# Kernel optimization log

Hardware: AMD Instinct MI355X
Metric: run time of the kernel (lower is better)

Reference implementation:

```python
import jax, jax.numpy as jnp
import numpy as np
from jax import lax

B, T, D, H = 2, 2048, 512, 8
HD = D // H
EPS = 1e-5


def _layernorm(x, g, b):
    m = jnp.mean(x, axis=-1, keepdims=True)
    v = jnp.var(x, axis=-1, keepdims=True)
    return (x - m) / jnp.sqrt(v + EPS) * g + b


def setup_inputs() -> dict:
    key = jax.random.key(0)
    ks = jax.random.split(key, 16)
    s = 0.02
    return {
        "x": jax.random.normal(ks[0], (B, T, D), jnp.float32),
        "pe": jax.random.normal(ks[1], (B, T, D), jnp.float32),
        "conv_w": jax.random.normal(ks[2], (D, D, 3), jnp.float32) * s,   # OIH
        "conv_b": jnp.zeros((D,), jnp.float32),
        "in_proj_w": jax.random.normal(ks[3], (3 * D, D), jnp.float32) * s,
        "in_proj_b": jnp.zeros((3 * D,), jnp.float32),
        "out_proj_w": jax.random.normal(ks[4], (D, D), jnp.float32) * s,
        "out_proj_b": jnp.zeros((D,), jnp.float32),
        "ln1_g": jnp.ones((D,), jnp.float32),
        "ln1_b": jnp.zeros((D,), jnp.float32),
        "w1": jax.random.normal(ks[5], (2 * D, D), jnp.float32) * s,
        "b1": jnp.zeros((2 * D,), jnp.float32),
        "w2": jax.random.normal(ks[6], (D, 2 * D), jnp.float32) * s,
        "b2": jnp.zeros((D,), jnp.float32),
        "ln2_g": jnp.ones((D,), jnp.float32),
        "ln2_b": jnp.zeros((D,), jnp.float32),
    }


def reference(x, pe, conv_w, conv_b, in_proj_w, in_proj_b, out_proj_w,
              out_proj_b, ln1_g, ln1_b, w1, b1, w2, b2, ln2_g, ln2_b):
    Bv, Tv, Dv = x.shape
    window = max(Tv // 4, 1)
    half = window // 2
    idx = jnp.arange(Tv)
    blocked = jnp.abs(idx[:, None] - idx[None, :]) > half  # [T, T]
    mask = jnp.where(blocked, -jnp.inf, 0.0).astype(x.dtype)

    # Conv1d on values: x [B,T,D] -> [B,D,T], kernel3 pad1, back to [B,T,D]
    xT = jnp.transpose(x, (0, 2, 1))
    v_in = lax.conv_general_dilated(xT, conv_w, window_strides=(1,),
                                    padding=((1, 1),),
                                    dimension_numbers=("NCH", "OIH", "NCH"))
    v_in = jnp.transpose(v_in + conv_b[None, :, None], (0, 2, 1))

    # MultiheadAttention(q=x, k=x, v=v_in)
    Wq, Wk, Wv = jnp.split(in_proj_w, 3, axis=0)
    bq, bk, bv = jnp.split(in_proj_b, 3, axis=0)
    q = (x @ Wq.T + bq).reshape(Bv, Tv, H, HD).transpose(0, 2, 1, 3)
    k = (x @ Wk.T + bk).reshape(Bv, Tv, H, HD).transpose(0, 2, 1, 3)
    v = (v_in @ Wv.T + bv).reshape(Bv, Tv, H, HD).transpose(0, 2, 1, 3)

    scores = jnp.einsum("bhqd,bhkd->bhqk", q, k) / np.sqrt(HD).astype(x.dtype)
    scores = scores + mask[None, None]
    attn = jax.nn.softmax(scores, axis=-1)
    ctx = jnp.einsum("bhqk,bhkd->bhqd", attn, v)
    ctx = ctx.transpose(0, 2, 1, 3).reshape(Bv, Tv, Dv)
    attn_out = ctx @ out_proj_w.T + out_proj_b

    h = _layernorm(x + attn_out, ln1_g, ln1_b)
    ffn = jax.nn.relu(h @ w1.T + b1) @ w2.T + b2
    return _layernorm(h + ffn, ln2_g, ln2_b)
```

## Files before the change

### kernel.cpp

```cpp
#include <hip/hip_runtime.h>
#include <cstdint>
#include <cstddef>

static constexpr int kT  = 2048;
static constexpr int kD  = 512;
static constexpr int kB  = 2;
static constexpr int kN  = kB * kT;

using short8 = __attribute__((ext_vector_type(8))) short;
using f32x4  = __attribute__((ext_vector_type(4))) float;
typedef unsigned short ushort;

__device__ inline ushort f2bf(float f) {
  uint32_t u = __builtin_bit_cast(uint32_t, f);
  uint32_t r = (u + 0x7FFFu + ((u >> 16) & 1u)) >> 16;
  return (ushort)r;
}

#define GLOAD_LDS16(g, l)                                         \
  __builtin_amdgcn_global_load_lds(                               \
      (const __attribute__((address_space(1))) void*)(g),         \
      (__attribute__((address_space(3))) void*)(l), 16, 0, 0)

__global__ __launch_bounds__(256) void cast_kernel(
    const float* __restrict__ in, ushort* __restrict__ out, int n4)
{
  for (int t = blockIdx.x * 256 + threadIdx.x; t < n4; t += gridDim.x * 256) {
    float4 v = *reinterpret_cast<const float4*>(&in[(size_t)t * 4]);
    ushort o[4] = {f2bf(v.x), f2bf(v.y), f2bf(v.z), f2bf(v.w)};
    *reinterpret_cast<uint2*>(&out[(size_t)t * 4]) =
        *reinterpret_cast<uint2*>(o);
  }
}

__global__ __launch_bounds__(256) void convw_kernel(
    const float* __restrict__ cw, ushort* __restrict__ wcat)
{
  for (int t = blockIdx.x * 256 + threadIdx.x; t < kD * kD;
       t += gridDim.x * 256) {
    int o = t >> 9, i = t & 511;
    const float* src = &cw[(size_t)(o * kD + i) * 3];
    ushort* dst = &wcat[(size_t)o * (3 * kD) + i];
#pragma unroll
    for (int tap = 0; tap < 3; ++tap) dst[tap * kD] = f2bf(src[tap]);
  }
}

__global__ __launch_bounds__(256) void acat_kernel(
    const ushort* __restrict__ xb, ushort* __restrict__ acat)
{
  const int total = kN * 3 * 64;
  for (int t = blockIdx.x * 256 + threadIdx.x; t < total;
       t += gridDim.x * 256) {
    int m = t / 192, r = t - m * 192;
    int tap = r >> 6, i8 = r & 63;
    int tib = (m & (kT - 1)) + tap - 1;
    uint4 v = {0u, 0u, 0u, 0u};
    if (tib >= 0 && tib < kT)
      v = *reinterpret_cast<const uint4*>(&xb[(size_t)(m + tap - 1) * kD + i8 * 8]);
    *reinterpret_cast<uint4*>(&acat[(size_t)m * (3 * kD) + tap * kD + i8 * 8]) = v;
  }
}

template <typename OutT, int RELU>
__global__ __launch_bounds__(256) void gemm_bf16(
    const ushort* __restrict__ A, const ushort* __restrict__ W,
    const float* __restrict__ bias, OutT* __restrict__ C,
    int M, int Nn, int K)
{
  __shared__ __align__(16) ushort As[2][64 * 64];
  __shared__ __align__(16) ushort Bs[2][64 * 64];
  const int tid = threadIdx.x;
  const int lane = tid & 63, w = tid >> 6;
  const int wr = w >> 1, wc = w & 1;
  const int m0 = blockIdx.x * 64, n0 = blockIdx.y * 64;
  const int fr = lane & 15, g = lane >> 4;

  f32x4 acc[2][2];
#pragma unroll
  for (int i = 0; i < 2; ++i)
#pragma unroll
    for (int j = 0; j < 2; ++j) acc[i][j] = {0.f, 0.f, 0.f, 0.f};

  const int u0 = tid, u1 = tid + 256;
  const int r0s = u0 >> 3, c0s = (u0 & 7) ^ (r0s & 7);
  const int r1s = u1 >> 3, c1s = (u1 & 7) ^ (r1s & 7);
  const ushort* gA0 = A + (size_t)(m0 + r0s) * K + c0s * 8;
  const ushort* gA1 = A + (size_t)(m0 + r1s) * K + c1s * 8;
  const ushort* gB0 = W + (size_t)(n0 + r0s) * K + c0s * 8;
  const ushort* gB1 = W + (size_t)(n0 + r1s) * K + c1s * 8;
  const int ld0 = w * 512;
  const int ld1 = 2048 + w * 512;

  auto stage = [&](int buf, int k0) {
    GLOAD_LDS16(gA0 + k0, &As[buf][ld0]);
    GLOAD_LDS16(gA1 + k0, &As[buf][ld1]);
    GLOAD_LDS16(gB0 + k0, &Bs[buf][ld0]);
    GLOAD_LDS16(gB1 + k0, &Bs[buf][ld1]);
  };

  const int nt = K >> 6;
  stage(0, 0);
  int cur = 0;
  for (int t = 0; t < nt; ++t) {
    if (t + 1 < nt) {
      stage(cur ^ 1, (t + 1) << 6);
      asm volatile("s_waitcnt vmcnt(4)" ::: "memory");
    } else {
      asm volatile("s_waitcnt vmcnt(0)" ::: "memory");
    }
    __builtin_amdgcn_s_barrier();
    __builtin_amdgcn_sched_barrier(0);

    short8 a[2][2], b[2][2];
#pragma unroll
    for (int m = 0; m < 2; ++m)
#pragma unroll
      for (int kc = 0; kc < 2; ++kc) {
        int r = wr * 32 + m * 16 + fr;
        a[m][kc] = *reinterpret_cast<const short8*>(
            &As[cur][r * 64 + (((kc * 4 + g) ^ (r & 7)) * 8)]);
      }
#pragma unroll
    for (int n = 0; n < 2; ++n)
#pragma unroll
      for (int kc = 0; kc < 2; ++kc) {
        int r = wc * 32 + n * 16 + fr;
        b[n][kc] = *reinterpret_cast<const short8*>(
            &Bs[cur][r * 64 + (((kc * 4 + g) ^ (r & 7)) * 8)]);
      }
#pragma unroll
    for (int m = 0; m < 2; ++m)
#pragma unroll
      for (int n = 0; n < 2; ++n)
#pragma unroll
        for (int kc = 0; kc < 2; ++kc)
          acc[m][n] = __builtin_amdgcn_mfma_f32_16x16x32_bf16(
              a[m][kc], b[n][kc], acc[m][n], 0, 0, 0);

    __builtin_amdgcn_sched_barrier(0);
    __builtin_amdgcn_s_barrier();
    cur ^= 1;
  }

  float bv[2];
#pragma unroll
  for (int n = 0; n < 2; ++n) bv[n] = bias[n0 + wc * 32 + n * 16 + fr];
#pragma unroll
  for (int m = 0; m < 2; ++m) {
#pragma unroll
    for (int j = 0; j < 4; ++j) {
      int row = m0 + wr * 32 + m * 16 + g * 4 + j;
#pragma unroll
      for (int n = 0; n < 2; ++n) {
        int col = n0 + wc * 32 + n * 16 + fr;
        float v = acc[m][n][j] + bv[n];
        if (RELU) v = fmaxf(v, 0.f);
        if constexpr (sizeof(OutT) == 2)
          C[(size_t)row * Nn + col] = (OutT)f2bf(v);
        else
          C[(size_t)row * Nn + col] = (OutT)v;
      }
    }
  }
}

__global__ __launch_bounds__(256) void attn_mfma(
    const ushort* __restrict__ QK, const ushort* __restrict__ V,
    ushort* __restrict__ Ctx)
{
  constexpr int PAD = 72;
  __shared__ __align__(16) ushort Ks[64 * 64];
  __shared__ __align__(16) ushort Vt[64][PAD];
  __shared__ __align__(16) ushort Pl[4][16][PAD];
  const int tid = threadIdx.x;
  const int lane = tid & 63, w = tid >> 6;
  const int l15 = lane & 15, g = lane >> 4;
  const int bh = blockIdx.y;
  const int b = bh >> 3, h = bh & 7;
  const int r0 = blockIdx.x * 64;
  const int rowbase = b * kT;
  const int qrow0 = r0 + w * 16;
  const int t_lo = max(r0 - 256, 0);
  const int t_last = min(r0 + 256, kT - 64);
  const int ntiles = ((t_last - t_lo) >> 6) + 1;

  short8 qf[2];
  {
    const size_t qb = (size_t)(rowbase + qrow0 + l15) * 1024 + h * 64 + g * 8;
    qf[0] = *reinterpret_cast<const short8*>(&QK[qb]);
    qf[1] = *reinterpret_cast<const short8*>(&QK[qb + 32]);
  }

  f32x4 acc[4];
#pragma unroll
  for (int d = 0; d < 4; ++d) acc[d] = {0.f, 0.f, 0.f, 0.f};
  float mrun[4] = {-1e30f, -1e30f, -1e30f, -1e30f};
  float lrun[4] = {0.f, 0.f, 0.f, 0.f};

  for (int tt = 0; tt < ntiles; ++tt) {
    const int j0 = t_lo + tt * 64;

#pragma unroll
    for (int c = 0; c < 2; ++c) {
      int u = c * 256 + tid;
      int row = u >> 3;
      int col8 = (u & 7) ^ (row & 7);
      const ushort* src =
          &QK[(size_t)(rowbase + j0 + row) * 1024 + 512 + h * 64 + col8 * 8];
      GLOAD_LDS16(src, &Ks[(c * 256 + w * 64) * 8]);
    }
#pragma unroll
    for (int i = 0; i < 2; ++i) {
      int dg = w + 4 * i;
      uint4 vv = *reinterpret_cast<const uint4*>(
          &V[(size_t)(rowbase + j0 + lane) * 512 + h * 64 + dg * 8]);
      ushort tmp[8];
      *reinterpret_cast<uint4*>(tmp) = vv;
#pragma unroll
      for (int e = 0; e < 8; ++e) Vt[dg * 8 + e][lane] = tmp[e];
    }
    __syncthreads();

    f32x4 s[4];
#pragma unroll
    for (int n = 0; n < 4; ++n) {
      f32x4 z = {0.f, 0.f, 0.f, 0.f};
#pragma unroll
      for (int kc = 0; kc < 2; ++kc) {
        int row = n * 16 + l15;
        int unit = row * 8 + ((kc * 4 + g) ^ (row & 7));
        short8 kb = *reinterpret_cast<const short8*>(&Ks[unit * 8]);
        z = __builtin_amdgcn_mfma_f32_16x16x32_bf16(qf[kc], kb, z, 0, 0, 0);
      }
      s[n] = z;
    }
#pragma unroll
    for (int n = 0; n < 4; ++n)
#pragma unroll
      for (int j = 0; j < 4; ++j) {
        int col = j0 + n * 16 + l15;
        int qr = qrow0 + g * 4 + j;
        int dlt = col - qr;
        float v = s[n][j] * 0.125f;
        s[n][j] = (dlt > 256 || dlt < -256) ? -1e30f : v;
      }
    float pn[4][4];
    float sold[4];
#pragma unroll
    for (int j = 0; j < 4; ++j) {
      float mx = fmaxf(fmaxf(s[0][j], s[1][j]), fmaxf(s[2][j], s[3][j]));
      mx = fmaxf(mx, __shfl_xor(mx, 1));
      mx = fmaxf(mx, __shfl_xor(mx, 2));
      mx = fmaxf(mx, __shfl_xor(mx, 4));
      mx = fmaxf(mx, __shfl_xor(mx, 8));
      float mnew = fmaxf(mrun[j], mx);
      float sc = __expf(mrun[j] - mnew);
      mrun[j] = mnew;
      sold[j] = sc;
      float rs = 0.f;
#pragma unroll
      for (int n = 0; n < 4; ++n) {
        float p = __expf(s[n][j] - mnew);
        pn[n][j] = p;
        rs += p;
      }
      rs += __shfl_xor(rs, 1);
      rs += __shfl_xor(rs, 2);
      rs += __shfl_xor(rs, 4);
      rs += __shfl_xor(rs, 8);
      lrun[j] = lrun[j] * sc + rs;
    }
#pragma unroll
    for (int d = 0; d < 4; ++d)
#pragma unroll
      for (int j = 0; j < 4; ++j) acc[d][j] *= sold[j];
#pragma unroll
    for (int n = 0; n < 4; ++n)
#pragma unroll
      for (int j = 0; j < 4; ++j)
        Pl[w][g * 4 + j][n * 16 + l15] = f2bf(pn[n][j]);
    asm volatile("s_waitcnt lgkmcnt(0)" ::: "memory");
    __builtin_amdgcn_sched_barrier(0);

    short8 pa[2];
    pa[0] = *reinterpret_cast<const short8*>(&Pl[w][l15][g * 8]);
    pa[1] = *reinterpret_cast<const short8*>(&Pl[w][l15][32 + g * 8]);
#pragma unroll
    for (int d = 0; d < 4; ++d) {
#pragma unroll
      for (int kc = 0; kc < 2; ++kc) {
        short8 vb = *reinterpret_cast<const short8*>(
            &Vt[d * 16 + l15][kc * 32 + g * 8]);
        acc[d] = __builtin_amdgcn_mfma_f32_16x16x32_bf16(pa[kc], vb, acc[d], 0, 0, 0);
      }
    }
    __syncthreads();
  }

  float inv[4];
#pragma unroll
  for (int j = 0; j < 4; ++j) inv[j] = 1.f / lrun[j];
#pragma unroll
  for (int d = 0; d < 4; ++d)
#pragma unroll
    for (int j = 0; j < 4; ++j) {
      float v = acc[d][j] * inv[j];
      Ctx[(size_t)(rowbase + qrow0 + g * 4 + j) * 512 + h * 64 + d * 16 + l15] =
          f2bf(v);
    }
}

__global__ __launch_bounds__(256) void ln_kernel(
    const float* __restrict__ A, const float* __restrict__ Bq,
    const float* __restrict__ G, const float* __restrict__ Bt,
    float* __restrict__ Out, ushort* __restrict__ OutB)
{
  const int lane = threadIdx.x & 63;
  const int wv = threadIdx.x >> 6;
  const int row = blockIdx.x * 4 + wv;
  const size_t base = (size_t)row * kD + lane * 8;

  float4 a0 = *reinterpret_cast<const float4*>(&A[base]);
  float4 a1 = *reinterpret_cast<const float4*>(&A[base + 4]);
  float4 b0 = *reinterpret_cast<const float4*>(&Bq[base]);
  float4 b1 = *reinterpret_cast<const float4*>(&Bq[base + 4]);
  float x[8] = {a0.x + b0.x, a0.y + b0.y, a0.z + b0.z, a0.w + b0.w,
                a1.x + b1.x, a1.y + b1.y, a1.z + b1.z, a1.w + b1.w};
  float s = 0.f, ss = 0.f;
#pragma unroll
  for (int i = 0; i < 8; ++i) { s += x[i]; ss += x[i] * x[i]; }
#pragma unroll
  for (int o = 1; o < 64; o <<= 1) {
    s += __shfl_xor(s, o, 64);
    ss += __shfl_xor(ss, o, 64);
  }
  const float mean = s * (1.f / kD);
  const float var = ss * (1.f / kD) - mean * mean;
  const float rs = rsqrtf(var + 1e-5f);

  const int c = lane * 8;
  float4 g0 = *reinterpret_cast<const float4*>(&G[c]);
  float4 g1 = *reinterpret_cast<const float4*>(&G[c + 4]);
  float4 t0 = *reinterpret_cast<const float4*>(&Bt[c]);
  float4 t1 = *reinterpret_cast<const float4*>(&Bt[c + 4]);
  float y[8];
  y[0] = (x[0] - mean) * rs * g0.x + t0.x;
  y[1] = (x[1] - mean) * rs * g0.y + t0.y;
  y[2] = (x[2] - mean) * rs * g0.z + t0.z;
  y[3] = (x[3] - mean) * rs * g0.w + t0.w;
  y[4] = (x[4] - mean) * rs * g1.x + t1.x;
  y[5] = (x[5] - mean) * rs * g1.y + t1.y;
  y[6] = (x[6] - mean) * rs * g1.z + t1.z;
  y[7] = (x[7] - mean) * rs * g1.w + t1.w;
  *reinterpret_cast<float4*>(&Out[base]) = {y[0], y[1], y[2], y[3]};
  *reinterpret_cast<float4*>(&Out[base + 4]) = {y[4], y[5], y[6], y[7]};
  if (OutB) {
    ushort ob[8];
#pragma unroll
    for (int i = 0; i < 8; ++i) ob[i] = f2bf(y[i]);
    *reinterpret_cast<uint4*>(&OutB[base]) = *reinterpret_cast<uint4*>(ob);
  }
}

extern "C" void kernel_launch(void* const* d_in, const int* in_sizes, int n_in,
                              void* d_out, int out_size, void* d_ws, size_t ws_size,
                              hipStream_t stream)
{
  const float* x   = (const float*)d_in[0];
  const float* cw  = (const float*)d_in[2];
  const float* cb  = (const float*)d_in[3];
  const float* ipw = (const float*)d_in[4];
  const float* ipb = (const float*)d_in[5];
  const float* opw = (const float*)d_in[6];
  const float* opb = (const float*)d_in[7];
  const float* g1  = (const float*)d_in[8];
  const float* b1n = (const float*)d_in[9];
  const float* w1  = (const float*)d_in[10];
  const float* bb1 = (const float*)d_in[11];
  const float* w2  = (const float*)d_in[12];
  const float* bb2 = (const float*)d_in[13];
  const float* g2  = (const float*)d_in[14];
  const float* b2n = (const float*)d_in[15];
  float* out = (float*)d_out;

  char* p = (char*)d_ws;
  auto take = [&](size_t bytes) {
    char* q = p; p += (bytes + 255) & ~size_t(255); return q;
  };
  ushort* xb    = (ushort*)take((size_t)kN * kD * 2);
  char*  acat_r =          take((size_t)kN * 3 * kD * 2);
  ushort* acat  = (ushort*)acat_r;
  ushort* wcat  = (ushort*)take((size_t)kD * 3 * kD * 2);
  ushort* ipwb  = (ushort*)take((size_t)3 * kD * kD * 2);
  ushort* opwb  = (ushort*)take((size_t)kD * kD * 2);
  ushort* w1b   = (ushort*)take((size_t)2 * kD * kD * 2);
  ushort* w2b   = (ushort*)take((size_t)2 * kD * kD * 2);
  ushort* convo = (ushort*)take((size_t)kN * kD * 2);
  char*  qk_r   =          take((size_t)kN * 2 * kD * 2);
  ushort* qkb   = (ushort*)qk_r;
  ushort* vbb   = (ushort*)take((size_t)kN * kD * 2);
  ushort* ctx   = (ushort*)take((size_t)kN * kD * 2);
  float* hbuf   = (float*)take((size_t)kN * kD * 4);
  ushort* hb    = (ushort*)take((size_t)kN * kD * 2);
  float* attno  = (float*)acat_r;
  ushort* f1    = (ushort*)qk_r;
  float* f2     = (float*)acat_r;

  dim3 blk(256);
  cast_kernel<<<dim3(1024), blk, 0, stream>>>(x, xb, kN * kD / 4);
  cast_kernel<<<dim3(512), blk, 0, stream>>>(ipw, ipwb, 3 * kD * kD / 4);
  cast_kernel<<<dim3(256), blk, 0, stream>>>(opw, opwb, kD * kD / 4);
  cast_kernel<<<dim3(512), blk, 0, stream>>>(w1, w1b, 2 * kD * kD / 4);
  cast_kernel<<<dim3(512), blk, 0, stream>>>(w2, w2b, 2 * kD * kD / 4);
  convw_kernel<<<dim3(1024), blk, 0, stream>>>(cw, wcat);
  acat_kernel<<<dim3(1024), blk, 0, stream>>>(xb, acat);

  gemm_bf16<ushort, 0><<<dim3(kN / 64, kD / 64), blk, 0, stream>>>(
      acat, wcat, cb, convo, kN, kD, 3 * kD);
  gemm_bf16<ushort, 0><<<dim3(kN / 64, 1024 / 64), blk, 0, stream>>>(
      xb, ipwb, ipb, qkb, kN, 1024, kD);
  gemm_bf16<ushort, 0><<<dim3(kN / 64, kD / 64), blk, 0, stream>>>(
      convo, ipwb + (size_t)1024 * kD, ipb + 1024, vbb, kN, kD, kD);
  attn_mfma<<<dim3(kT / 64, kB * 8), blk, 0, stream>>>(qkb, vbb, ctx);
  gemm_bf16<float, 0><<<dim3(kN / 64, kD / 64), blk, 0, stream>>>(
      ctx, opwb, opb, attno, kN, kD, kD);
  ln_kernel<<<dim3(kN / 4), blk, 0, stream>>>(x, attno, g1, b1n, hbuf, hb);
  gemm_bf16<ushort, 1><<<dim3(kN / 64, 1024 / 64), blk, 0, stream>>>(
      hb, w1b, bb1, f1, kN, 1024, kD);
  gemm_bf16<float, 0><<<dim3(kN / 64, kD / 64), blk, 0, stream>>>(
      f1, w2b, bb2, f2, kN, kD, 2 * kD);
  ln_kernel<<<dim3(kN / 4), blk, 0, stream>>>(hbuf, f2, g2, b2n, out, nullptr);
}
```

Measured before the change: 214.3 us.

## Fuse prep casts into one kernel and triple-buffer GEMM LDS

Merges seven small conversion launches (activation/weight bf16 casts, conv weight reshape, im2col-style acat build) into a single prep kernel, and builds acat directly from the fp32 input so it no longer waits on the xb cast. This removes launch overhead and serialization between tiny kernels. The GEMM moves from double to triple LDS buffering with a two-tile prefetch distance, deepening the load pipeline. In exchange, LDS use per block grows, which may reduce occupancy.

```diff
diff --git a/kernel.cpp b/kernel.cpp
--- a/kernel.cpp
+++ b/kernel.cpp
@@ -22,43 +22,66 @@
       (const __attribute__((address_space(1))) void*)(g),         \
       (__attribute__((address_space(3))) void*)(l), 16, 0, 0)
 
-__global__ __launch_bounds__(256) void cast_kernel(
-    const float* __restrict__ in, ushort* __restrict__ out, int n4)
+__global__ __launch_bounds__(256) void prep_kernel(
+    const float* __restrict__ x,   const float* __restrict__ ipw,
+    const float* __restrict__ opw, const float* __restrict__ w1,
+    const float* __restrict__ w2,  const float* __restrict__ cw,
+    ushort* __restrict__ xb,   ushort* __restrict__ ipwb,
+    ushort* __restrict__ opwb, ushort* __restrict__ w1b,
+    ushort* __restrict__ w2b,  ushort* __restrict__ wcat,
+    ushort* __restrict__ acat)
 {
-  for (int t = blockIdx.x * 256 + threadIdx.x; t < n4; t += gridDim.x * 256) {
-    float4 v = *reinterpret_cast<const float4*>(&in[(size_t)t * 4]);
+  constexpr int C0 = 524288;
+  constexpr int C1 = C0 + 196608;
+  constexpr int C2 = C1 + 65536;
+  constexpr int C3 = C2 + 131072;
+  constexpr int C4 = C3 + 131072;
+  constexpr int C5 = C4 + 262144;
+  constexpr int C6 = C5 + 786432;
+
+  auto cast4 = [](const float* in, ushort* out, int u) {
+    float4 v = *reinterpret_cast<const float4*>(&in[(size_t)u * 4]);
     ushort o[4] = {f2bf(v.x), f2bf(v.y), f2bf(v.z), f2bf(v.w)};
-    *reinterpret_cast<uint2*>(&out[(size_t)t * 4]) =
+    *reinterpret_cast<uint2*>(&out[(size_t)u * 4]) =
         *reinterpret_cast<uint2*>(o);
-  }
-}
-
-__global__ __launch_bounds__(256) void convw_kernel(
-    const float* __restrict__ cw, ushort* __restrict__ wcat)
-{
-  for (int t = blockIdx.x * 256 + threadIdx.x; t < kD * kD;
-       t += gridDim.x * 256) {
-    int o = t >> 9, i = t & 511;
-    const float* src = &cw[(size_t)(o * kD + i) * 3];
-    ushort* dst = &wcat[(size_t)o * (3 * kD) + i];
-#pragma unroll
-    for (int tap = 0; tap < 3; ++tap) dst[tap * kD] = f2bf(src[tap]);
-  }
-}
-
-__global__ __launch_bounds__(256) void acat_kernel(
-    const ushort* __restrict__ xb, ushort* __restrict__ acat)
-{
-  const int total = kN * 3 * 64;
-  for (int t = blockIdx.x * 256 + threadIdx.x; t < total;
-       t += gridDim.x * 256) {
-    int m = t / 192, r = t - m * 192;
-    int tap = r >> 6, i8 = r & 63;
-    int tib = (m & (kT - 1)) + tap - 1;
-    uint4 v = {0u, 0u, 0u, 0u};
-    if (tib >= 0 && tib < kT)
-      v = *reinterpret_cast<const uint4*>(&xb[(size_t)(m + tap - 1) * kD + i8 * 8]);
-    *reinterpret_cast<uint4*>(&acat[(size_t)m * (3 * kD) + tap * kD + i8 * 8]) = v;
+  };
+
+  for (int u = blockIdx.x * 256 + threadIdx.x; u < C6; u += gridDim.x * 256) {
+    if (u < C0) {
+      cast4(x, xb, u);
+    } else if (u < C1) {
+      cast4(ipw, ipwb, u - C0);
+    } else if (u < C2) {
+      cast4(opw, opwb, u - C1);
+    } else if (u < C3) {
+      cast4(w1, w1b, u - C2);
+    } else if (u < C4) {
+      cast4(w2, w2b, u - C3);
+    } else if (u < C5) {
+      int t = u - C4;
+      int o = t >> 9, i = t & 511;
+      const float* src = &cw[(size_t)(o * kD + i) * 3];
+      ushort* dst = &wcat[(size_t)o * (3 * kD) + i];
+#pragma unroll
+      for (int tap = 0; tap < 3; ++tap) dst[tap * kD] = f2bf(src[tap]);
+    } else {
+      int t = u - C5;
+      int m = t / 192, r = t - m * 192;
+      int tap = r >> 6, i8 = r & 63;
+      int tib = (m & (kT - 1)) + tap - 1;
+      ushort ob[8] = {0, 0, 0, 0, 0, 0, 0, 0};
+      if (tib >= 0 && tib < kT) {
+        const float* src = &x[(size_t)(m + tap - 1) * kD + i8 * 8];
+        float4 v0 = *reinterpret_cast<const float4*>(src);
+        float4 v1 = *reinterpret_cast<const float4*>(src + 4);
+        ob[0] = f2bf(v0.x); ob[1] = f2bf(v0.y); ob[2] = f2bf(v0.z);
+        ob[3] = f2bf(v0.w); ob[4] = f2bf(v1.x); ob[5] = f2bf(v1.y);
+        ob[6] = f2bf(v1.z); ob[7] = f2bf(v1.w);
+      }
+      *reinterpret_cast<uint4*>(
+          &acat[(size_t)m * (3 * kD) + tap * kD + i8 * 8]) =
+          *reinterpret_cast<uint4*>(ob);
+    }
   }
 }
 
@@ -68,8 +91,8 @@
     const float* __restrict__ bias, OutT* __restrict__ C,
     int M, int Nn, int K)
 {
-  __shared__ __align__(16) ushort As[2][64 * 64];
-  __shared__ __align__(16) ushort Bs[2][64 * 64];
+  __shared__ __align__(16) ushort As[3][64 * 64];
+  __shared__ __align__(16) ushort Bs[3][64 * 64];
   const int tid = threadIdx.x;
   const int lane = tid & 63, w = tid >> 6;
   const int wr = w >> 1, wc = w & 1;
@@ -101,10 +124,13 @@
 
   const int nt = K >> 6;
   stage(0, 0);
-  int cur = 0;
+  stage(1, 64);
+  int cur = 0, b2 = 2;
   for (int t = 0; t < nt; ++t) {
-    if (t + 1 < nt) {
-      stage(cur ^ 1, (t + 1) << 6);
+    if (t + 2 < nt) {
+      stage(b2, (t + 2) << 6);
+      asm volatile("s_waitcnt vmcnt(8)" ::: "memory");
+    } else if (t + 1 < nt) {
       asm volatile("s_waitcnt vmcnt(4)" ::: "memory");
     } else {
       asm volatile("s_waitcnt vmcnt(0)" ::: "memory");
@@ -140,7 +166,8 @@
 
     __builtin_amdgcn_sched_barrier(0);
     __builtin_amdgcn_s_barrier();
-    cur ^= 1;
+    cur = cur == 2 ? 0 : cur + 1;
+    b2 = b2 == 2 ? 0 : b2 + 1;
   }
 
   float bv[2];
@@ -408,13 +435,8 @@
   float* f2     = (float*)acat_r;
 
   dim3 blk(256);
-  cast_kernel<<<dim3(1024), blk, 0, stream>>>(x, xb, kN * kD / 4);
-  cast_kernel<<<dim3(512), blk, 0, stream>>>(ipw, ipwb, 3 * kD * kD / 4);
-  cast_kernel<<<dim3(256), blk, 0, stream>>>(opw, opwb, kD * kD / 4);
-  cast_kernel<<<dim3(512), blk, 0, stream>>>(w1, w1b, 2 * kD * kD / 4);
-  cast_kernel<<<dim3(512), blk, 0, stream>>>(w2, w2b, 2 * kD * kD / 4);
-  convw_kernel<<<dim3(1024), blk, 0, stream>>>(cw, wcat);
-  acat_kernel<<<dim3(1024), blk, 0, stream>>>(xb, acat);
+  prep_kernel<<<dim3(2048), blk, 0, stream>>>(
+      x, ipw, opw, w1, w2, cw, xb, ipwb, opwb, w1b, w2b, wcat, acat);
 
   gemm_bf16<ushort, 0><<<dim3(kN / 64, kD / 64), blk, 0, stream>>>(
       acat, wcat, cb, convo, kN, kD, 3 * kD);
```

Result: no change. 210.9 us (-1.6%).
